# Kernel optimization log

Hardware: AMD Instinct MI355X
Metric: run time of the kernel (lower is better)

## Reference

```python
import jax, jax.numpy as jnp
import numpy as np

D_MODEL = 1024
NHEAD = 16
D_K = D_MODEL // NHEAD  # 64
B, L = 2, 2048


def _apply_rotary(x, cos, sin):
    # x: (B, H, L, d_k); cos/sin: (B, L, d_k//2)
    d_half = x.shape[-1] // 2
    x1, x2 = x[..., :d_half], x[..., d_half:]
    c = cos[:, None, :, :]
    s = sin[:, None, :, :]
    return jnp.concatenate([x1 * c - x2 * s, x1 * s + x2 * c], axis=-1)


def setup_inputs() -> dict:
    key = jax.random.key(0)
    ks = jax.random.split(key, 7)
    x = jax.random.normal(ks[0], (B, L, D_MODEL), dtype=jnp.float32)
    rope_cos = jax.random.uniform(ks[1], (B, L, D_K // 2), dtype=jnp.float32)
    rope_sin = jax.random.uniform(ks[2], (B, L, D_K // 2), dtype=jnp.float32)
    # Linear params (PyTorch layout: weight (out, in), y = x @ W.T + b)
    lim_qkv = 1.0 / np.sqrt(D_MODEL)
    W_qkv = jax.random.uniform(ks[3], (3 * D_MODEL, D_MODEL), dtype=jnp.float32, minval=-lim_qkv, maxval=lim_qkv)
    b_qkv = jax.random.uniform(ks[4], (3 * D_MODEL,), dtype=jnp.float32, minval=-lim_qkv, maxval=lim_qkv)
    W_out = jax.random.uniform(ks[5], (D_MODEL, D_MODEL), dtype=jnp.float32, minval=-lim_qkv, maxval=lim_qkv)
    b_out = jax.random.uniform(ks[6], (D_MODEL,), dtype=jnp.float32, minval=-lim_qkv, maxval=lim_qkv)
    return {"x": x, "rope_cos": rope_cos, "rope_sin": rope_sin,
            "W_qkv": W_qkv, "b_qkv": b_qkv, "W_out": W_out, "b_out": b_out}


def reference(x, rope_cos, rope_sin, W_qkv, b_qkv, W_out, b_out):
    Bx, Lx, D = x.shape
    scale = D_K ** -0.5
    qkv = x @ W_qkv.T + b_qkv                     # (B, L, 3D)
    qkv = qkv.reshape(Bx, Lx, 3, NHEAD, D_K)
    q = jnp.transpose(qkv[:, :, 0], (0, 2, 1, 3))  # (B, H, L, d_k)
    k = jnp.transpose(qkv[:, :, 1], (0, 2, 1, 3))
    v = jnp.transpose(qkv[:, :, 2], (0, 2, 1, 3))
    q = _apply_rotary(q, rope_cos, rope_sin)
    k = _apply_rotary(k, rope_cos, rope_sin)
    attn = jnp.einsum("bhqd,bhkd->bhqk", q, k) * scale  # (B, H, L, L)
    attn = jax.nn.softmax(attn, axis=-1)
    out = jnp.einsum("bhqk,bhkd->bhqd", attn, v)          # (B, H, L, d_k)
    out = jnp.transpose(out, (0, 2, 1, 3)).reshape(Bx, Lx, D)
    return out @ W_out.T + b_out
```

## Files before the change

### kernel.cpp

```cpp
#include <hip/hip_runtime.h>
#include <hip/hip_bf16.h>
#include <stdint.h>


typedef __attribute__((ext_vector_type(8)))  short bf16x8;
typedef __attribute__((ext_vector_type(4)))  float f32x4;
typedef __attribute__((ext_vector_type(16))) float f32x16;
typedef __attribute__((ext_vector_type(4)))  short short4v;
typedef __attribute__((ext_vector_type(4)))  unsigned int u32x4;

#define DEV static __device__ __forceinline__

DEV short f2bf(float f) {
  uint32_t u = __builtin_bit_cast(uint32_t, f);
  u += 0x7FFFu + ((u >> 16) & 1u);
  return (short)(u >> 16);
}
DEV float bf2f(short s) {
  return __builtin_bit_cast(float, ((uint32_t)(uint16_t)s) << 16);
}
DEV uint32_t pkbf(float a, float b) {
  __hip_bfloat162 h = __float22bfloat162_rn(make_float2(a, b));
  uint32_t u;
  __builtin_memcpy(&u, &h, 4);
  return u;
}
DEV void pl32swap(uint32_t &dst, uint32_t &src) {
  asm volatile("v_permlane32_swap_b32 %0, %1" : "+v"(dst), "+v"(src));
}

#define AS1 __attribute__((address_space(1)))
#define AS3 __attribute__((address_space(3)))
#define GLOAD_LDS16(gp, lp) \
  __builtin_amdgcn_global_load_lds((const AS1 void*)(gp), (AS3 void*)(lp), 16, 0, 0)

__global__ void k_cvt_bf16(const float* __restrict__ in, short* __restrict__ out, int n4) {
  int i = blockIdx.x * 256 + threadIdx.x;
  if (i >= n4) return;
  float4 v = reinterpret_cast<const float4*>(in)[i];
  short4v o = { f2bf(v.x), f2bf(v.y), f2bf(v.z), f2bf(v.w) };
  reinterpret_cast<short4v*>(out)[i] = o;
}

#define GEMM_BODY(A_, Bt_, K_)                                              \
  __shared__ short Lds[2 * 128 * 64];                                       \
  short* As = Lds;                                                          \
  short* Bs = Lds + 128 * 64;                                               \
  const int tid = threadIdx.x;                                              \
  const int lane = tid & 63;                                                \
  const int wid  = tid >> 6;                                                \
  const int lq = lane & 15, lg = lane >> 4;                                 \
  const int wr = wid >> 1, wc = wid & 1;                                    \
  const int m0 = blockIdx.y * 128;                                          \
  const int n0 = blockIdx.x * 128;                                          \
  f32x4 acc[4][4];                                                          \
  _Pragma("unroll")                                                         \
  for (int i = 0; i < 4; ++i)                                               \
    _Pragma("unroll")                                                       \
    for (int j = 0; j < 4; ++j) acc[i][j] = (f32x4){0.f, 0.f, 0.f, 0.f};    \
  const int KT = (K_) >> 6;                                                 \
  for (int kt = 0; kt < KT; ++kt) {                                         \
    const short* Ag = (A_)  + (size_t)m0 * (K_) + kt * 64;                  \
    const short* Bg = (Bt_) + (size_t)n0 * (K_) + kt * 64;                  \
    _Pragma("unroll")                                                       \
    for (int p = 0; p < 4; ++p) {                                           \
      int f = p * 256 + tid;                                                \
      int row = f >> 3;                                                     \
      int sch = (f & 7) ^ (row & 7);            \
      GLOAD_LDS16(Ag + (size_t)row * (K_) + sch * 8, As + f * 8);           \
      GLOAD_LDS16(Bg + (size_t)row * (K_) + sch * 8, Bs + f * 8);           \
    }                                                                       \
    asm volatile("s_waitcnt vmcnt(0)" ::: "memory");                        \
    __syncthreads();                                                        \
    _Pragma("unroll")                                                       \
    for (int kk = 0; kk < 2; ++kk) {                                        \
      bf16x8 af[4], bfr[4];                                                 \
      _Pragma("unroll")                                                     \
      for (int i = 0; i < 4; ++i)                                           \
        af[i]  = *reinterpret_cast<const bf16x8*>(                          \
            &As[(wr*64 + i*16 + lq) * 64 + (((kk*4 + lg) ^ (lq & 7)) * 8)]);\
      _Pragma("unroll")                                                     \
      for (int j = 0; j < 4; ++j)                                           \
        bfr[j] = *reinterpret_cast<const bf16x8*>(                          \
            &Bs[(wc*64 + j*16 + lq) * 64 + (((kk*4 + lg) ^ (lq & 7)) * 8)]);\
      _Pragma("unroll")                                                     \
      for (int i = 0; i < 4; ++i)                                           \
        _Pragma("unroll")                                                   \
        for (int j = 0; j < 4; ++j)                                         \
          acc[i][j] = __builtin_amdgcn_mfma_f32_16x16x32_bf16(              \
              af[i], bfr[j], acc[i][j], 0, 0, 0);                           \
    }                                                                       \
    __syncthreads();                                                        \
  }

__global__ __launch_bounds__(256) void k_gemm_qkv(
    const short* __restrict__ A, const short* __restrict__ Bt,
    const float* __restrict__ bias,
    const float* __restrict__ cosb, const float* __restrict__ sinb,
    short* __restrict__ Qb, short* __restrict__ Kb, short* __restrict__ Vt)
{
  GEMM_BODY(A, Bt, 1024)

  short* Ep = Lds + wid * 4096;
  const int cglob = n0 + wc * 64;
  if (cglob < 2048) {
    const bool isq = (cglob < 1024);
    const float QS = isq ? 0.125f * 1.4426950408889634f : 1.0f;
    short* dst = isq ? Qb : Kb;
    const int h = (cglob & 1023) >> 6;
    const float b0 = bias[cglob + lq],      b2 = bias[cglob + 32 + lq];
    const float b1 = bias[cglob + 16 + lq], b3 = bias[cglob + 48 + lq];
    #pragma unroll
    for (int i = 0; i < 4; ++i) {
      #pragma unroll
      for (int r = 0; r < 4; ++r) {
        int lloc = i*16 + lg*4 + r;
        int rg = m0 + wr*64 + lloc;
        float c0 = cosb[(size_t)rg * 32 + lq];
        float s0 = sinb[(size_t)rg * 32 + lq];
        float c1 = cosb[(size_t)rg * 32 + 16 + lq];
        float s1 = sinb[(size_t)rg * 32 + 16 + lq];
        float x1 = acc[i][0][r] + b0, x2 = acc[i][2][r] + b2;
        Ep[lloc*64 + lq]      = f2bf((x1 * c0 - x2 * s0) * QS);
        Ep[lloc*64 + 32 + lq] = f2bf((x1 * s0 + x2 * c0) * QS);
        float y1 = acc[i][1][r] + b1, y2 = acc[i][3][r] + b3;
        Ep[lloc*64 + 16 + lq] = f2bf((y1 * c1 - y2 * s1) * QS);
        Ep[lloc*64 + 48 + lq] = f2bf((y1 * s1 + y2 * c1) * QS);
      }
    }
    #pragma unroll
    for (int p = 0; p < 8; ++p) {
      int f = p * 64 + lane;
      int lloc = f >> 3, d0 = (f & 7) * 8;
      int rg = m0 + wr*64 + lloc;
      int bi = rg >> 11, ll = rg & 2047;
      bf16x8 v = *reinterpret_cast<const bf16x8*>(&Ep[lloc*64 + d0]);
      *reinterpret_cast<bf16x8*>(
          &dst[((size_t)(bi * 16 + h) * 2048 + ll) * 64 + d0]) = v;
    }
  } else {
    const int h = (cglob - 2048) >> 6;
    #pragma unroll
    for (int i = 0; i < 4; ++i) {
      int lloc = i*16 + lg*4;
      #pragma unroll
      for (int j = 0; j < 4; ++j) {
        int d = j * 16 + lq;
        float bv = bias[cglob + d];
        short4v pk4 = { f2bf(acc[i][j][0] + bv), f2bf(acc[i][j][1] + bv),
                        f2bf(acc[i][j][2] + bv), f2bf(acc[i][j][3] + bv) };
        *reinterpret_cast<short4v*>(
            &Ep[d*64 + (lloc ^ ((d & 7) << 3))]) = pk4;
      }
    }
    #pragma unroll
    for (int p = 0; p < 8; ++p) {
      int f = p * 64 + lane;
      int d = f >> 3, lc = (f & 7) * 8;
      bf16x8 v = *reinterpret_cast<const bf16x8*>(&Ep[d*64 + lc]);
      int lreal = lc ^ ((d & 7) << 3);
      int rg = m0 + wr*64 + lreal;
      int bi = rg >> 11, ll = rg & 2047;
      *reinterpret_cast<bf16x8*>(
          &Vt[((size_t)(bi * 16 + h) * 64 + d) * 2048 + ll]) = v;
    }
  }
}

__global__ __launch_bounds__(256) void k_gemm_out(
    const short* __restrict__ A, const short* __restrict__ Bt,
    const float* __restrict__ bias, float* __restrict__ C)
{
  GEMM_BODY(A, Bt, 1024)
  const int N = 1024;
  #pragma unroll
  for (int i = 0; i < 4; ++i) {
    int rbase = m0 + wr*64 + i*16 + lg*4;
    #pragma unroll
    for (int j = 0; j < 4; ++j) {
      int col = n0 + wc*64 + j*16 + lq;
      float bv = bias[col];
      #pragma unroll
      for (int r = 0; r < 4; ++r)
        C[(size_t)(rbase + r) * N + col] = acc[i][j][r] + bv;
    }
  }
}

__global__ __launch_bounds__(256, 4) void k_attn(
    const short* __restrict__ Q, const short* __restrict__ Kb,
    const short* __restrict__ Vt,
    short* __restrict__ P0, short* __restrict__ P1,
    float* __restrict__ L0, float* __restrict__ L1)
{
  __shared__ short Ks[2][64 * 64];
  __shared__ short Vs[2][64 * 64];
  const int tid = threadIdx.x;
  const int lane = tid & 63;
  const int wid  = tid >> 6;
  const int Lq = lane & 31;
  const int h  = lane >> 5;
  const int bh = blockIdx.y;
  const int q0 = blockIdx.x * 128 + wid * 32;
  const int b = bh >> 4, hh = bh & 15;
  const int t0 = blockIdx.z * 16;
  short* Pp = blockIdx.z ? P1 : P0;
  float* Lp = blockIdx.z ? L1 : L0;

  const short* Qp = Q  + ((size_t)bh * 2048 + q0 + Lq) * 64;
  const short* Kp = Kb + (size_t)bh * 2048 * 64;
  const short* Vp = Vt + (size_t)bh * 64 * 2048;

  #define STAGE_KV(c, t) do {                                              \
    const short* Kg_ = Kp + (size_t)(t) * 64 * 64;                         \
    const short* Vg_ = Vp + (size_t)(t) * 64;                              \
    _Pragma("unroll")                                                      \
    for (int p_ = 0; p_ < 2; ++p_) {                                       \
      int f_ = p_ * 256 + tid;                                             \
      int row_ = f_ >> 3;                                                  \
      int sch_ = (f_ & 7) ^ (row_ & 7);                                    \
      GLOAD_LDS16(Kg_ + row_ * 64 + sch_ * 8,            &Ks[c][f_ * 8]);  \
      GLOAD_LDS16(Vg_ + (size_t)row_ * 2048 + sch_ * 8,  &Vs[c][f_ * 8]);  \
    }                                                                      \
  } while (0)

  bf16x8 qf[4];
  #pragma unroll
  for (int ks = 0; ks < 4; ++ks)
    qf[ks] = *reinterpret_cast<const bf16x8*>(Qp + ks * 16 + h * 8);

  f32x16 o[2];
  #pragma unroll
  for (int nd = 0; nd < 2; ++nd)
    #pragma unroll
    for (int r = 0; r < 16; ++r) o[nd][r] = 0.f;
  float la0 = 0.f, la1 = 0.f;

  STAGE_KV(0, t0);
  asm volatile("s_waitcnt vmcnt(0)" ::: "memory");
  __syncthreads();

  for (int kk2 = 0; kk2 < 16; ++kk2) {
    const int cur = kk2 & 1;
    if (kk2 < 15) STAGE_KV(cur ^ 1, t0 + kk2 + 1);

    #pragma unroll
    for (int mb = 0; mb < 2; ++mb) {
      f32x16 sm;
      #pragma unroll
      for (int r = 0; r < 16; ++r) sm[r] = 0.f;
      #pragma unroll
      for (int ks = 0; ks < 4; ++ks) {
        bf16x8 kf = *reinterpret_cast<const bf16x8*>(
            &Ks[cur][(mb*32 + Lq) * 64 + (((ks*2 + h) ^ (Lq & 7)) * 8)]);
        sm = __builtin_amdgcn_mfma_f32_32x32x16_bf16(kf, qf[ks], sm, 0, 0, 0);
      }
      #pragma unroll
      for (int half = 0; half < 2; ++half) {
        float e0 = __builtin_amdgcn_exp2f(sm[8*half + 0]);
        float e1 = __builtin_amdgcn_exp2f(sm[8*half + 1]);
        float e2 = __builtin_amdgcn_exp2f(sm[8*half + 2]);
        float e3 = __builtin_amdgcn_exp2f(sm[8*half + 3]);
        float e4 = __builtin_amdgcn_exp2f(sm[8*half + 4]);
        float e5 = __builtin_amdgcn_exp2f(sm[8*half + 5]);
        float e6 = __builtin_amdgcn_exp2f(sm[8*half + 6]);
        float e7 = __builtin_amdgcn_exp2f(sm[8*half + 7]);
        la0 += (e0 + e1) + (e4 + e5);
        la1 += (e2 + e3) + (e6 + e7);
        uint32_t w0 = pkbf(e0, e1), w1 = pkbf(e2, e3);
        uint32_t w2 = pkbf(e4, e5), w3 = pkbf(e6, e7);
        pl32swap(w0, w2);
        pl32swap(w1, w3);
        u32x4 paw = { w0, w1, w2, w3 };
        bf16x8 pa = __builtin_bit_cast(bf16x8, paw);
        const int ksl = mb * 2 + half;
        #pragma unroll
        for (int nd = 0; nd < 2; ++nd) {
          bf16x8 vf = *reinterpret_cast<const bf16x8*>(
              &Vs[cur][(nd*32 + Lq) * 64 + (((ksl*2 + h) ^ (Lq & 7)) * 8)]);
          o[nd] = __builtin_amdgcn_mfma_f32_32x32x16_bf16(pa, vf, o[nd], 0, 0, 0);
        }
      }
    }
    asm volatile("s_waitcnt vmcnt(0)" ::: "memory");
    __syncthreads();
  }

  float l_part = la0 + la1;
  l_part += __shfl_xor(l_part, 32, 64);
  if (h == 0) Lp[((size_t)bh << 11) + q0 + Lq] = l_part;
  #pragma unroll
  for (int r = 0; r < 16; ++r) {
    int qrow = (r & 3) + 8 * (r >> 2) + 4 * h;
    size_t rowb = ((size_t)b * 2048 + q0 + qrow) * 1024 + hh * 64;
    Pp[rowb + Lq]      = f2bf(o[0][r]);
    Pp[rowb + 32 + Lq] = f2bf(o[1][r]);
  }
  #undef STAGE_KV
}

__global__ void k_merge(const short* __restrict__ P0, const short* __restrict__ P1,
                        const float* __restrict__ L0, const float* __restrict__ L1,
                        short* __restrict__ AO)
{
  int idx = blockIdx.x * 256 + threadIdx.x;
  int rg = idx >> 7;
  int c0 = (idx & 127) * 8;
  int bh = ((rg >> 11) << 4) + (c0 >> 6);
  size_t lix = ((size_t)bh << 11) + (rg & 2047);
  float inv = 1.f / (L0[lix] + L1[lix]);
  size_t off = (size_t)rg * 1024 + c0;
  bf16x8 a = *reinterpret_cast<const bf16x8*>(&P0[off]);
  bf16x8 bv = *reinterpret_cast<const bf16x8*>(&P1[off]);
  bf16x8 r;
  #pragma unroll
  for (int j = 0; j < 8; ++j)
    r[j] = f2bf((bf2f(a[j]) + bf2f(bv[j])) * inv);
  *reinterpret_cast<bf16x8*>(&AO[off]) = r;
}

extern "C" void kernel_launch(void* const* d_in, const int* in_sizes, int n_in,
                              void* d_out, int out_size, void* d_ws, size_t ws_size,
                              hipStream_t stream) {
  (void)in_sizes; (void)n_in; (void)out_size; (void)ws_size;
  const float* x    = (const float*)d_in[0];
  const float* rc   = (const float*)d_in[1];
  const float* rs   = (const float*)d_in[2];
  const float* Wqkv = (const float*)d_in[3];
  const float* bqkv = (const float*)d_in[4];
  const float* Wout = (const float*)d_in[5];
  const float* bout = (const float*)d_in[6];
  float* out = (float*)d_out;

  char* ws = (char*)d_ws;
  short* xb  = (short*)(ws);
  short* wqb = (short*)(ws + 8388608);
  short* wob = (short*)(ws + 14680064);
  short* Qb  = (short*)(ws + 16777216);
  short* Kb  = (short*)(ws + 25165824);
  short* Vt  = (short*)(ws + 33554432);
  short* P0  = (short*)(ws + 41943040);
  short* P1  = (short*)(ws + 50331648);
  float* L0  = (float*)(ws + 58720256);
  float* L1  = (float*)(ws + 58982400);

  k_cvt_bf16<<<4096, 256, 0, stream>>>(x,    xb,  1048576);
  k_cvt_bf16<<<3072, 256, 0, stream>>>(Wqkv, wqb, 786432);
  k_cvt_bf16<<<1024, 256, 0, stream>>>(Wout, wob, 262144);
  k_gemm_qkv<<<dim3(24, 32), 256, 0, stream>>>(xb, wqb, bqkv, rc, rs, Qb, Kb, Vt);
  k_attn<<<dim3(16, 32, 2), 256, 0, stream>>>(Qb, Kb, Vt, P0, P1, L0, L1);
  k_merge<<<2048, 256, 0, stream>>>(P0, P1, L0, L1, P0);
  k_gemm_out<<<dim3(8, 32), 256, 0, stream>>>(P0, wob, bout, out);
}
```

Measured before the change: 132.8 us.

## Double-buffer GEMM LDS tiles to prefetch the next K-slice during MFMA compute

The shared GEMM body now uses two LDS buffer pairs. It issues the async global-to-LDS loads for tile kt+1 before running the MFMAs on tile kt, so load latency overlaps with compute instead of waiting on vmcnt(0) every iteration. This doubles the LDS footprint to 64 KB per block, which may lower occupancy. The explicit s_waitcnt was removed, so correctness now depends on __syncthreads also waiting for the outstanding LDS-DMA loads.

```diff
diff --git a/kernel.cpp b/kernel.cpp
--- a/kernel.cpp
+++ b/kernel.cpp
@@ -42,10 +42,20 @@
   reinterpret_cast<short4v*>(out)[i] = o;
 }
 
+DEV void gemm_stage(const short* Ag, const short* Bg, int K_,
+                    short* AsD, short* BsD, int tid) {
+  #pragma unroll
+  for (int p = 0; p < 4; ++p) {
+    int f = p * 256 + tid;
+    int row = f >> 3;
+    int sch = (f & 7) ^ (row & 7);
+    GLOAD_LDS16(Ag + (size_t)row * K_ + sch * 8, AsD + f * 8);
+    GLOAD_LDS16(Bg + (size_t)row * K_ + sch * 8, BsD + f * 8);
+  }
+}
+
 #define GEMM_BODY(A_, Bt_, K_)                                              \
-  __shared__ short Lds[2 * 128 * 64];                                       \
-  short* As = Lds;                                                          \
-  short* Bs = Lds + 128 * 64;                                               \
+  __shared__ short Lds[4 * 128 * 64];    \
   const int tid = threadIdx.x;                                              \
   const int lane = tid & 63;                                                \
   const int wid  = tid >> 6;                                                \
@@ -59,19 +69,18 @@
     _Pragma("unroll")                                                       \
     for (int j = 0; j < 4; ++j) acc[i][j] = (f32x4){0.f, 0.f, 0.f, 0.f};    \
   const int KT = (K_) >> 6;                                                 \
+  gemm_stage((A_) + (size_t)m0 * (K_), (Bt_) + (size_t)n0 * (K_), (K_),     \
+             Lds, Lds + 8192, tid);                                         \
+  __syncthreads();                                                          \
+  int gbuf = 0;                                                             \
   for (int kt = 0; kt < KT; ++kt) {                                         \
-    const short* Ag = (A_)  + (size_t)m0 * (K_) + kt * 64;                  \
-    const short* Bg = (Bt_) + (size_t)n0 * (K_) + kt * 64;                  \
-    _Pragma("unroll")                                                       \
-    for (int p = 0; p < 4; ++p) {                                           \
-      int f = p * 256 + tid;                                                \
-      int row = f >> 3;                                                     \
-      int sch = (f & 7) ^ (row & 7);            \
-      GLOAD_LDS16(Ag + (size_t)row * (K_) + sch * 8, As + f * 8);           \
-      GLOAD_LDS16(Bg + (size_t)row * (K_) + sch * 8, Bs + f * 8);           \
-    }                                                                       \
-    asm volatile("s_waitcnt vmcnt(0)" ::: "memory");                        \
-    __syncthreads();                                                        \
+    if (kt + 1 < KT)                                                        \
+      gemm_stage((A_)  + (size_t)m0 * (K_) + (kt + 1) * 64,                 \
+                 (Bt_) + (size_t)n0 * (K_) + (kt + 1) * 64, (K_),           \
+                 Lds + (gbuf ^ 1) * 16384,                                  \
+                 Lds + (gbuf ^ 1) * 16384 + 8192, tid);                     \
+    const short* As = Lds + gbuf * 16384;                                   \
+    const short* Bs = As + 8192;                                            \
     _Pragma("unroll")                                                       \
     for (int kk = 0; kk < 2; ++kk) {                                        \
       bf16x8 af[4], bfr[4];                                                 \
@@ -91,6 +100,7 @@
               af[i], bfr[j], acc[i][j], 0, 0, 0);                           \
     }                                                                       \
     __syncthreads();                                                        \
+    gbuf ^= 1;                                                              \
   }
 
 __global__ __launch_bounds__(256) void k_gemm_qkv(
```

After: 120.0 us. -9.6%, faster.
